# Kernel optimization log

Hardware: AMD Instinct MI355X
Metric: run time of the kernel (lower is better)

## Reference

```python
import jax, jax.numpy as jnp
import numpy as np

B, S, M = 8, 2048, 2048
STATE, MEM, DH, DOUT = 1024, 1024, 512, 512
K_CURV = 1.0
BETA = 1.0 / np.sqrt(DH)
EPS = 1e-12
MAX_TAN_NORM = 3.5


def setup_inputs() -> dict:
    key = jax.random.key(0)
    ks = jax.random.split(key, 6)
    return {
        "queries": jax.random.normal(ks[0], (B, S, STATE), jnp.float32),
        "keys": jax.random.normal(ks[1], (B, M, MEM), jnp.float32),
        "values": jax.random.normal(ks[2], (B, M, MEM), jnp.float32),
        "Wq": jax.random.normal(ks[3], (DH, STATE), jnp.float32) * (1.0 / np.sqrt(STATE)),
        "bq": jnp.zeros((DH,), jnp.float32),
        "Wk": jax.random.normal(ks[4], (DH, MEM), jnp.float32) * (1.0 / np.sqrt(MEM)),
        "bk": jnp.zeros((DH,), jnp.float32),
        "Wv": jax.random.normal(ks[5], (DOUT, MEM), jnp.float32) * (1.0 / np.sqrt(MEM)),
        "bv": jnp.zeros((DOUT,), jnp.float32),
    }


def _expmap0(x, k):
    # to_tangent0: [0, x] with norm clamped to <= 3.5 (time component is 0 so norm == ||x||)
    n = jnp.linalg.norm(x, axis=-1, keepdims=True)
    v = x * jnp.minimum(MAX_TAN_NORM / (n + 1e-7), 1.0)
    # exp map at origin o = (1/sqrt(k), 0) of Lorentz model with <x,x>_L = -1/k
    sk = jnp.sqrt(k)
    vn = jnp.maximum(jnp.linalg.norm(v, axis=-1, keepdims=True), EPS)
    th = sk * vn
    x0 = jnp.cosh(th) / sk
    xs = jnp.sinh(th) * v / (sk * vn)
    return jnp.concatenate([x0, xs], axis=-1)  # (..., d+1)


def _forward(queries, keys, values, Wq, bq, Wk, bk, Wv, bv):
    k = jnp.asarray(K_CURV, queries.dtype)
    sk = jnp.sqrt(k)
    Q = _expmap0(queries @ Wq.T + bq, k)  # (B,S,DH+1)
    Kh = _expmap0(keys @ Wk.T + bk, k)    # (B,M,DH+1)
    V = _expmap0(values @ Wv.T + bv, k)   # (B,M,DOUT+1)

    # pairwise Lorentz distance: d(x,y) = arccosh(-k <x,y>_L)/sqrt(k)
    # <x,y>_L = -x0*y0 + xs.ys ; computed as matmul + rank-1 term, no (B,S,M,d) blowup
    inner = jnp.einsum('bsd,bmd->bsm', Q[..., 1:], Kh[..., 1:]) \
            - Q[..., 0][:, :, None] * Kh[..., 0][:, None, :]
    dists = jnp.arccosh(jnp.maximum(-k * inner, 1.0 + 1e-7)) / sk  # (B,S,M)

    alpha = jax.nn.softmax(-BETA * dists, axis=-1)  # (B,S,M)

    # Einstein midpoint aggregation
    v_klein = V[..., 1:] / jnp.maximum(V[..., :1], EPS)                 # (B,M,DOUT)
    vn2 = jnp.minimum(jnp.sum(v_klein * v_klein, -1, keepdims=True), 1.0 - 1e-6)
    gamma = 1.0 / jnp.sqrt(jnp.maximum(1.0 - vn2, EPS))                 # (B,M,1)
    denom = jnp.maximum(jnp.einsum('bsm,bm->bs', alpha, gamma[..., 0]), EPS)[..., None]
    mid = jnp.einsum('bsm,bmd->bsd', alpha, gamma * v_klein) / denom    # (B,S,DOUT)
    mn = jnp.maximum(jnp.linalg.norm(mid, axis=-1, keepdims=True), EPS)
    mid = jnp.where(mn >= 1.0, mid / mn * (1.0 - 1e-6), mid)

    # Klein -> hyperboloid
    mn2 = jnp.minimum(jnp.sum(mid * mid, -1, keepdims=True), 1.0 - 1e-6)
    z0 = 1.0 / jnp.sqrt(jnp.maximum(k * (1.0 - mn2), EPS))
    zs = z0 * mid

    # logmap0 -> Euclidean spatial components
    d0 = jnp.arccosh(jnp.maximum(sk * z0, 1.0 + 1e-7)) / sk
    zsn = jnp.maximum(jnp.linalg.norm(zs, axis=-1, keepdims=True), EPS)
    return d0 * zs / zsn  # (B,S,DOUT)


def reference(queries, keys, values, Wq, bq, Wk, bk, Wv, bv):
    return _forward(queries, keys, values, Wq, bq, Wk, bk, Wv, bv)
```

## Files before the change

kernel.cpp:

```cpp
#include <hip/hip_runtime.h>
#include <hip/hip_bf16.h>
#include <cstdint>
#include <cstddef>


typedef _Float16 f16x8 __attribute__((ext_vector_type(8)));
typedef _Float16 f16x4 __attribute__((ext_vector_type(4)));
typedef float    f32x4 __attribute__((ext_vector_type(4)));

#define BETA_F 0.04419417382415922f
#define LOG2E_F 1.4426950408889634f
#define LN2_F 0.6931471805599453f

__device__ __forceinline__ void gload_lds16(const void* g, void* l) {
  __builtin_amdgcn_global_load_lds(
      (__attribute__((address_space(1))) void*)(g),
      (__attribute__((address_space(3))) void*)(l), 16, 0, 0);
}

#define K1_PIT 40

__global__ __launch_bounds__(256) void k_proj(
    const float* __restrict__ xq, const float* __restrict__ xk, const float* __restrict__ xv,
    const float* __restrict__ wq, const float* __restrict__ wk, const float* __restrict__ wv,
    const float* __restrict__ bq, const float* __restrict__ bk, const float* __restrict__ bv,
    _Float16* __restrict__ proj)
{
  __shared__ __align__(16) _Float16 As[128 * K1_PIT];
  __shared__ __align__(16) _Float16 Bs[128 * K1_PIT];

  const int tid = threadIdx.x;
  const int w = tid >> 6, l = tid & 63, ln = l & 15, q = l >> 4;
  const int wm = w & 1, wn = w >> 1;
  const int r0 = blockIdx.y * 128;
  const int n0 = blockIdx.x * 128;
  const int which = r0 >> 14;
  const int rloc = r0 & 16383;
  const float* X = (which == 0) ? xq : ((which == 1) ? xk : xv);
  const float* W = (which == 0) ? wq : ((which == 1) ? wk : wv);
  const float* bias = (which == 0) ? bq : ((which == 1) ? bk : bv);

  f32x4 acc[4][4];
#pragma unroll
  for (int mt = 0; mt < 4; ++mt)
#pragma unroll
    for (int nt = 0; nt < 4; ++nt) acc[mt][nt] = f32x4{0.f, 0.f, 0.f, 0.f};

  for (int kk = 0; kk < 1024; kk += 32) {
    __syncthreads();
#pragma unroll
    for (int it = 0; it < 4; ++it) {
      int v = tid + 256 * it;
      int row = v >> 3, c4 = v & 7;
      float4 a = *(const float4*)(X + (size_t)(rloc + row) * 1024 + kk + c4 * 4);
      float4 b = *(const float4*)(W + (size_t)(n0 + row) * 1024 + kk + c4 * 4);
      f16x4 ah = { (_Float16)a.x, (_Float16)a.y, (_Float16)a.z, (_Float16)a.w };
      f16x4 bh = { (_Float16)b.x, (_Float16)b.y, (_Float16)b.z, (_Float16)b.w };
      *(f16x4*)&As[row * K1_PIT + c4 * 4] = ah;
      *(f16x4*)&Bs[row * K1_PIT + c4 * 4] = bh;
    }
    __syncthreads();

    f16x8 af[4], bf[4];
#pragma unroll
    for (int mt = 0; mt < 4; ++mt)
      af[mt] = *(const f16x8*)&As[(wm * 64 + mt * 16 + ln) * K1_PIT + q * 8];
#pragma unroll
    for (int nt = 0; nt < 4; ++nt)
      bf[nt] = *(const f16x8*)&Bs[(wn * 64 + nt * 16 + ln) * K1_PIT + q * 8];
#pragma unroll
    for (int mt = 0; mt < 4; ++mt)
#pragma unroll
      for (int nt = 0; nt < 4; ++nt)
        acc[mt][nt] = __builtin_amdgcn_mfma_f32_16x16x32_f16(af[mt], bf[nt], acc[mt][nt], 0, 0, 0);
  }

  float bl[4];
#pragma unroll
  for (int nt = 0; nt < 4; ++nt) bl[nt] = bias[n0 + wn * 64 + nt * 16 + ln];
#pragma unroll
  for (int mt = 0; mt < 4; ++mt)
#pragma unroll
    for (int nt = 0; nt < 4; ++nt)
#pragma unroll
      for (int i = 0; i < 4; ++i) {
        int r = r0 + wm * 64 + mt * 16 + q * 4 + i;
        int c = n0 + wn * 64 + nt * 16 + ln;
        proj[(size_t)r * 512 + c] = (_Float16)(acc[mt][nt][i] + bl[nt]);
      }
}

__global__ __launch_bounds__(256) void k_rowstats(
    const _Float16* __restrict__ proj, float* __restrict__ fs, float* __restrict__ c0)
{
  const int w = threadIdx.x >> 6, l = threadIdx.x & 63;
  const int r = blockIdx.x * 4 + w;
  const f16x8 v = *(const f16x8*)(proj + (size_t)r * 512 + l * 8);
  float ss = 0.f;
#pragma unroll
  for (int j = 0; j < 8; ++j) { float x = (float)v[j]; ss += x * x; }
#pragma unroll
  for (int m = 1; m < 64; m <<= 1) ss += __shfl_xor(ss, m, 64);
  if (l == 0) {
    float n = sqrtf(ss);
    float s = fminf(3.5f / (n + 1e-7f), 1.0f);
    float vn = fmaxf(n * s, 1e-12f);
    float e = __builtin_amdgcn_exp2f(vn * LOG2E_F);
    float ie = 1.0f / e;
    c0[r] = 0.5f * (e + ie);
    fs[r] = 0.5f * (e - ie) * s / vn;
  }
}

#define K2_TP 72

__global__ __launch_bounds__(256) void k_transpose_v(
    const _Float16* __restrict__ proj, _Float16* __restrict__ xvT)
{
  __shared__ __align__(16) unsigned short t[64 * K2_TP];
  const int b = blockIdx.z, m0 = blockIdx.x * 64, d0 = blockIdx.y * 64;
  const unsigned short* pv =
      (const unsigned short*)(proj + (size_t)(32768 + b * 2048 + m0) * 512);
#pragma unroll
  for (int it = 0; it < 2; ++it) {
    int v = threadIdx.x + 256 * it;
    int r = v >> 3, c4 = v & 7;
    uint4 dd = *(const uint4*)(pv + (size_t)r * 512 + d0 + c4 * 8);
    *(uint4*)&t[r * K2_TP + c4 * 8] = dd;
  }
  __syncthreads();
#pragma unroll
  for (int it = 0; it < 2; ++it) {
    int v = threadIdx.x + 256 * it;
    int dr = v >> 3, mc = v & 7;
    unsigned int o[4];
#pragma unroll
    for (int jj = 0; jj < 4; ++jj) {
      unsigned int lo = t[(mc * 8 + jj * 2) * K2_TP + dr];
      unsigned int hi = t[(mc * 8 + jj * 2 + 1) * K2_TP + dr];
      o[jj] = lo | (hi << 16);
    }
    uint4 dd = { o[0], o[1], o[2], o[3] };
    unsigned short* dst =
        (unsigned short*)(xvT + ((size_t)b * 512 + d0 + dr) * 2048 + m0 + mc * 8);
    *(uint4*)dst = dd;
  }
}

__global__ __launch_bounds__(256, 2) void k_attn(
    const _Float16* __restrict__ proj, const _Float16* __restrict__ xvT,
    const float* __restrict__ fs, const float* __restrict__ c0,
    float* __restrict__ out)
{
  __shared__ __align__(16) _Float16 KV[16384];
  __shared__ __align__(16) _Float16 P[32 * 40];
  __shared__ float s_den[2][32];
  __shared__ float s_mn2[4][32];
  __shared__ float s_g[32];

  const int tid = threadIdx.x;
  const int w = tid >> 6, l = tid & 63, ln = l & 15, q = l >> 4;
  const int rh = w >> 1, ch = w & 1;
  const int b = blockIdx.y;
  const int s0 = blockIdx.x * 32;

  const _Float16* projq = proj + (size_t)(b * 2048 + s0) * 512;
  const _Float16* projk = proj + (size_t)(16384 + b * 2048) * 512;
  const _Float16* vt = xvT + (size_t)b * 512 * 2048;
  const float* fqp = fs + b * 2048 + s0;
  const float* fkp = fs + 16384 + b * 2048;
  const float* fvp = fs + 32768 + b * 2048;
  const float* cqp = c0 + b * 2048 + s0;
  const float* ckp = c0 + 16384 + b * 2048;
  const float* cvp = c0 + 32768 + b * 2048;

  f16x8 qf[16];
  {
    const _Float16* qrow = projq + (size_t)(rh * 16 + ln) * 512;
#pragma unroll
    for (int kc = 0; kc < 16; ++kc) qf[kc] = *(const f16x8*)(qrow + kc * 32 + q * 8);
  }
  float cq_i[4], fq_i[4];
#pragma unroll
  for (int i = 0; i < 4; ++i) {
    cq_i[i] = cqp[rh * 16 + q * 4 + i];
    fq_i[i] = fqp[rh * 16 + q * 4 + i];
  }

  f32x4 acc[2][8];
#pragma unroll
  for (int rt = 0; rt < 2; ++rt)
#pragma unroll
    for (int nt = 0; nt < 8; ++nt) acc[rt][nt] = f32x4{0.f, 0.f, 0.f, 0.f};
  float den_acc[4] = {0.f, 0.f, 0.f, 0.f};

  for (int m0 = 0; m0 < 2048; m0 += 32) {
    __syncthreads();
#pragma unroll
    for (int rr = 0; rr < 8; ++rr) {
      int mloc = w * 8 + rr;
      const _Float16* g = projk + (size_t)(m0 + mloc) * 512 + ((l ^ (mloc & 7)) * 8);
      gload_lds16(g, &KV[mloc * 512]);
    }
    const int mla = m0 + ch * 16 + ln;
    const float ck_v = ckp[mla], fk_v = fkp[mla], fv_v = fvp[mla], cv_v = cvp[mla];
    __syncthreads();

    f32x4 pacc = f32x4{0.f, 0.f, 0.f, 0.f};
    {
      const _Float16* krow = &KV[(ch * 16 + ln) * 512];
      const int msw = (ch * 16 + ln) & 7;
#pragma unroll
      for (int kc = 0; kc < 16; ++kc) {
        f16x8 kf = *(const f16x8*)(krow + (((kc * 4 + q) ^ msw) * 8));
        pacc = __builtin_amdgcn_mfma_f32_16x16x32_f16(qf[kc], kf, pacc, 0, 0, 0);
      }
    }
#pragma unroll
    for (int i = 0; i < 4; ++i) {
      float x = cq_i[i] * ck_v - (fq_i[i] * fk_v) * pacc[i];
      x = fmaxf(x, 1.0f + 1e-7f);
      float r_ = x + __builtin_amdgcn_sqrtf(x * x - 1.0f);
      float p = __builtin_amdgcn_exp2f(-BETA_F * __builtin_amdgcn_logf(r_));
      den_acc[i] += p * cv_v;
      P[(rh * 16 + q * 4 + i) * 40 + ch * 16 + ln] = (_Float16)(p * fv_v);
    }
    __syncthreads();
#pragma unroll
    for (int uu = 0; uu < 8; ++uu) {
      int u = w * 8 + uu;
      int dloc = u * 16 + (l >> 2);
      int cg = (l & 3) ^ ((dloc >> 1) & 3);
      const _Float16* g = vt + (size_t)dloc * 2048 + m0 + cg * 8;
      gload_lds16(g, &KV[u * 512]);
    }
    __syncthreads();
#pragma unroll
    for (int rt = 0; rt < 2; ++rt) {
      f16x8 pf = *(const f16x8*)&P[(rt * 16 + ln) * 40 + q * 8];
#pragma unroll
      for (int nt = 0; nt < 8; ++nt) {
        int d = w * 128 + nt * 16 + ln;
        f16x8 vf = *(const f16x8*)&KV[d * 32 + ((q ^ ((d >> 1) & 3)) * 8)];
        acc[rt][nt] = __builtin_amdgcn_mfma_f32_16x16x32_f16(pf, vf, acc[rt][nt], 0, 0, 0);
      }
    }
  }

#pragma unroll
  for (int i = 0; i < 4; ++i) {
    float v = den_acc[i];
    v += __shfl_xor(v, 1, 64); v += __shfl_xor(v, 2, 64);
    v += __shfl_xor(v, 4, 64); v += __shfl_xor(v, 8, 64);
    if (ln == 0) s_den[ch][rh * 16 + q * 4 + i] = v;
  }
  __syncthreads();
  if (tid < 32) {
    float dv = fmaxf(s_den[0][tid] + s_den[1][tid], 1e-12f);
    s_den[0][tid] = 1.0f / dv;
  }
  __syncthreads();
#pragma unroll
  for (int rt = 0; rt < 2; ++rt)
#pragma unroll
    for (int i = 0; i < 4; ++i) {
      int s = rt * 16 + q * 4 + i;
      float inv = s_den[0][s];
      float mm = 0.f;
#pragma unroll
      for (int nt = 0; nt < 8; ++nt) {
        float mid = acc[rt][nt][i] * inv;
        mm += mid * mid;
      }
      mm += __shfl_xor(mm, 1, 64); mm += __shfl_xor(mm, 2, 64);
      mm += __shfl_xor(mm, 4, 64); mm += __shfl_xor(mm, 8, 64);
      if (ln == 0) s_mn2[w][s] = mm;
    }
  __syncthreads();
  if (tid < 32) {
    float mn2 = s_mn2[0][tid] + s_mn2[1][tid] + s_mn2[2][tid] + s_mn2[3][tid];
    float mn = sqrtf(mn2);
    float sc = (mn >= 1.0f) ? (1.0f - 1e-6f) / mn : 1.0f;
    float mn2c = fminf(mn2 * sc * sc, 1.0f - 1e-6f);
    float z0 = 1.0f / sqrtf(fmaxf(1.0f - mn2c, 1e-12f));
    float zc = fmaxf(z0, 1.0f + 1e-7f);
    float d0 = LN2_F * __builtin_amdgcn_logf(zc + __builtin_amdgcn_sqrtf(zc * zc - 1.0f));
    s_g[tid] = (d0 / fmaxf(mn, 1e-12f)) * s_den[0][tid];
  }
  __syncthreads();

  float* pbuf = (float*)KV;
  for (int sp = 0; sp < 16; ++sp) {
#pragma unroll
    for (int rt = 0; rt < 2; ++rt)
#pragma unroll
      for (int i = 0; i < 4; ++i) {
        int s = rt * 16 + q * 4 + i;
        if ((s >> 1) == sp) {
          float gg = s_g[s];
#pragma unroll
          for (int nt = 0; nt < 8; ++nt)
            pbuf[(s & 1) * 512 + w * 128 + nt * 16 + ln] = gg * acc[rt][nt][i];
        }
      }
    __syncthreads();
    {
      int row = tid >> 7, c4 = tid & 127;
      float4 vv = *(float4*)&pbuf[row * 512 + c4 * 4];
      *(float4*)&out[((size_t)(b * 2048 + s0 + sp * 2 + row)) * 512 + c4 * 4] = vv;
    }
    __syncthreads();
  }
}

extern "C" void kernel_launch(void* const* d_in, const int* in_sizes, int n_in,
                              void* d_out, int out_size, void* d_ws, size_t ws_size,
                              hipStream_t stream) {
  (void)in_sizes; (void)n_in; (void)out_size; (void)ws_size;
  const float* xq = (const float*)d_in[0];
  const float* xk = (const float*)d_in[1];
  const float* xv = (const float*)d_in[2];
  const float* wq = (const float*)d_in[3];
  const float* bq = (const float*)d_in[4];
  const float* wk = (const float*)d_in[5];
  const float* bk = (const float*)d_in[6];
  const float* wv = (const float*)d_in[7];
  const float* bv = (const float*)d_in[8];
  float* out = (float*)d_out;
  char* ws = (char*)d_ws;

  _Float16* proj = (_Float16*)(ws);
  _Float16* xvT  = (_Float16*)(ws + 50331648);
  float* fsc     = (float*)(ws + 67108864);
  float* c0a     = (float*)(ws + 67305472);

  k_proj<<<dim3(4, 384), 256, 0, stream>>>(xq, xk, xv, wq, wk, wv, bq, bk, bv, proj);
  k_rowstats<<<dim3(12288), 256, 0, stream>>>(proj, fsc, c0a);
  k_transpose_v<<<dim3(32, 8, 8), 256, 0, stream>>>(proj, xvT);
  k_attn<<<dim3(64, 8), 256, 0, stream>>>(proj, xvT, fsc, c0a, out);
}
```

Baseline: 479.6 us.

## Restructure projection and attention kernels with fp16 weights and fused row stats

A separate kernel now casts the weight matrices to fp16 once. The projection kernel uses 512 threads per block to cover all 512 output columns of a 128-row tile. It loads weights into LDS asynchronously with an XOR swizzle and computes the row norms and expmap coefficients in its epilogue, which removes the separate rowstats kernel. The attention kernel processes 64 keys per iteration with each wave owning 16 keys across both query subtiles, reads K and V fragments straight from global memory instead of staging them in LDS, double-buffers the P tile, and packs the coefficients as float2. The aim is fewer launches, less fp32 weight traffic and fewer barriers, at the cost of uncoalesced direct global reads for K and V.

```diff
diff --git a/kernel.cpp b/kernel.cpp
--- a/kernel.cpp
+++ b/kernel.cpp
@@ -18,97 +18,120 @@
       (__attribute__((address_space(3))) void*)(l), 16, 0, 0);
 }
 
-#define K1_PIT 40
-
-__global__ __launch_bounds__(256) void k_proj(
+__global__ __launch_bounds__(256) void k_wcast(
+    const float* __restrict__ wq, const float* __restrict__ wk,
+    const float* __restrict__ wv, _Float16* __restrict__ Wh)
+{
+  const int a = blockIdx.y;
+  const float* src = (a == 0) ? wq : ((a == 1) ? wk : wv);
+  const int idx = (blockIdx.x * 256 + threadIdx.x) * 8;
+  float4 v0 = *(const float4*)(src + idx);
+  float4 v1 = *(const float4*)(src + idx + 4);
+  f16x8 h = { (_Float16)v0.x, (_Float16)v0.y, (_Float16)v0.z, (_Float16)v0.w,
+              (_Float16)v1.x, (_Float16)v1.y, (_Float16)v1.z, (_Float16)v1.w };
+  *(f16x8*)(Wh + (size_t)a * 524288 + idx) = h;
+}
+
+#define APIT 72
+
+__global__ __launch_bounds__(512, 2) void k_proj(
     const float* __restrict__ xq, const float* __restrict__ xk, const float* __restrict__ xv,
-    const float* __restrict__ wq, const float* __restrict__ wk, const float* __restrict__ wv,
+    const _Float16* __restrict__ Wh,
     const float* __restrict__ bq, const float* __restrict__ bk, const float* __restrict__ bv,
-    _Float16* __restrict__ proj)
+    _Float16* __restrict__ proj, float2* __restrict__ fc2)
 {
-  __shared__ __align__(16) _Float16 As[128 * K1_PIT];
-  __shared__ __align__(16) _Float16 Bs[128 * K1_PIT];
+  __shared__ __align__(16) _Float16 As[128 * APIT];
+  __shared__ __align__(16) _Float16 Bs[512 * 64];
+  __shared__ float ssq[128];
 
   const int tid = threadIdx.x;
   const int w = tid >> 6, l = tid & 63, ln = l & 15, q = l >> 4;
   const int wm = w & 1, wn = w >> 1;
-  const int r0 = blockIdx.y * 128;
-  const int n0 = blockIdx.x * 128;
+  const int r0 = blockIdx.x * 128;
   const int which = r0 >> 14;
   const int rloc = r0 & 16383;
   const float* X = (which == 0) ? xq : ((which == 1) ? xk : xv);
-  const float* W = (which == 0) ? wq : ((which == 1) ? wk : wv);
+  const _Float16* Whb = Wh + (size_t)which * 524288;
   const float* bias = (which == 0) ? bq : ((which == 1) ? bk : bv);
 
-  f32x4 acc[4][4];
+  if (tid < 128) ssq[tid] = 0.f;
+
+  f32x4 acc[4][8];
 #pragma unroll
   for (int mt = 0; mt < 4; ++mt)
 #pragma unroll
-    for (int nt = 0; nt < 4; ++nt) acc[mt][nt] = f32x4{0.f, 0.f, 0.f, 0.f};
-
-  for (int kk = 0; kk < 1024; kk += 32) {
-    __syncthreads();
-#pragma unroll
-    for (int it = 0; it < 4; ++it) {
-      int v = tid + 256 * it;
-      int row = v >> 3, c4 = v & 7;
-      float4 a = *(const float4*)(X + (size_t)(rloc + row) * 1024 + kk + c4 * 4);
-      float4 b = *(const float4*)(W + (size_t)(n0 + row) * 1024 + kk + c4 * 4);
-      f16x4 ah = { (_Float16)a.x, (_Float16)a.y, (_Float16)a.z, (_Float16)a.w };
-      f16x4 bh = { (_Float16)b.x, (_Float16)b.y, (_Float16)b.z, (_Float16)b.w };
-      *(f16x4*)&As[row * K1_PIT + c4 * 4] = ah;
-      *(f16x4*)&Bs[row * K1_PIT + c4 * 4] = bh;
-    }
-    __syncthreads();
-
-    f16x8 af[4], bf[4];
-#pragma unroll
-    for (int mt = 0; mt < 4; ++mt)
-      af[mt] = *(const f16x8*)&As[(wm * 64 + mt * 16 + ln) * K1_PIT + q * 8];
-#pragma unroll
-    for (int nt = 0; nt < 4; ++nt)
-      bf[nt] = *(const f16x8*)&Bs[(wn * 64 + nt * 16 + ln) * K1_PIT + q * 8];
-#pragma unroll
-    for (int mt = 0; mt < 4; ++mt)
-#pragma unroll
-      for (int nt = 0; nt < 4; ++nt)
-        acc[mt][nt] = __builtin_amdgcn_mfma_f32_16x16x32_f16(af[mt], bf[nt], acc[mt][nt], 0, 0, 0);
-  }
-
-  float bl[4];
-#pragma unroll
-  for (int nt = 0; nt < 4; ++nt) bl[nt] = bias[n0 + wn * 64 + nt * 16 + ln];
+    for (int nt = 0; nt < 8; ++nt) acc[mt][nt] = f32x4{0.f, 0.f, 0.f, 0.f};
+
+  const int arow = tid >> 2, akq = tid & 3;
+  for (int kk = 0; kk < 1024; kk += 64) {
+    __syncthreads();
+    {
+      const float* xp = X + (size_t)(rloc + arow) * 1024 + kk + akq * 16;
+      float4 a0 = *(const float4*)(xp);
+      float4 a1 = *(const float4*)(xp + 4);
+      float4 a2 = *(const float4*)(xp + 8);
+      float4 a3 = *(const float4*)(xp + 12);
+      f16x8 h0 = { (_Float16)a0.x, (_Float16)a0.y, (_Float16)a0.z, (_Float16)a0.w,
+                   (_Float16)a1.x, (_Float16)a1.y, (_Float16)a1.z, (_Float16)a1.w };
+      f16x8 h1 = { (_Float16)a2.x, (_Float16)a2.y, (_Float16)a2.z, (_Float16)a2.w,
+                   (_Float16)a3.x, (_Float16)a3.y, (_Float16)a3.z, (_Float16)a3.w };
+      *(f16x8*)&As[arow * APIT + akq * 16] = h0;
+      *(f16x8*)&As[arow * APIT + akq * 16 + 8] = h1;
+    }
+#pragma unroll
+    for (int j = 0; j < 8; ++j) {
+      int u = w * 8 + j;
+      int row = u * 8 + (l >> 3);
+      int cg = (l & 7) ^ (row & 7);
+      gload_lds16(Whb + (size_t)row * 1024 + kk + cg * 8, &Bs[u * 512]);
+    }
+    __syncthreads();
+#pragma unroll
+    for (int kc = 0; kc < 2; ++kc) {
+      f16x8 af[4], bf[8];
+#pragma unroll
+      for (int mt = 0; mt < 4; ++mt)
+        af[mt] = *(const f16x8*)&As[(wm * 64 + mt * 16 + ln) * APIT + kc * 32 + q * 8];
+#pragma unroll
+      for (int nt = 0; nt < 8; ++nt) {
+        int row = wn * 128 + nt * 16 + ln;
+        bf[nt] = *(const f16x8*)&Bs[row * 64 + (((kc * 4 + q) ^ (row & 7)) * 8)];
+      }
+#pragma unroll
+      for (int mt = 0; mt < 4; ++mt)
+#pragma unroll
+        for (int nt = 0; nt < 8; ++nt)
+          acc[mt][nt] = __builtin_amdgcn_mfma_f32_16x16x32_f16(af[mt], bf[nt], acc[mt][nt], 0, 0, 0);
+    }
+  }
+
+  float bl[8];
+#pragma unroll
+  for (int nt = 0; nt < 8; ++nt) bl[nt] = bias[wn * 128 + nt * 16 + ln];
 #pragma unroll
   for (int mt = 0; mt < 4; ++mt)
 #pragma unroll
-    for (int nt = 0; nt < 4; ++nt)
-#pragma unroll
-      for (int i = 0; i < 4; ++i) {
-        int r = r0 + wm * 64 + mt * 16 + q * 4 + i;
-        int c = n0 + wn * 64 + nt * 16 + ln;
-        proj[(size_t)r * 512 + c] = (_Float16)(acc[mt][nt][i] + bl[nt]);
-      }
-}
-
-__global__ __launch_bounds__(256) void k_rowstats(
-    const _Float16* __restrict__ proj, float* __restrict__ fs, float* __restrict__ c0)
-{
-  const int w = threadIdx.x >> 6, l = threadIdx.x & 63;
-  const int r = blockIdx.x * 4 + w;
-  const f16x8 v = *(const f16x8*)(proj + (size_t)r * 512 + l * 8);
-  float ss = 0.f;
-#pragma unroll
-  for (int j = 0; j < 8; ++j) { float x = (float)v[j]; ss += x * x; }
-#pragma unroll
-  for (int m = 1; m < 64; m <<= 1) ss += __shfl_xor(ss, m, 64);
-  if (l == 0) {
-    float n = sqrtf(ss);
+    for (int i = 0; i < 4; ++i) {
+      float ss = 0.f;
+#pragma unroll
+      for (int nt = 0; nt < 8; ++nt) {
+        float v = acc[mt][nt][i] + bl[nt];
+        proj[(size_t)(r0 + wm * 64 + mt * 16 + q * 4 + i) * 512 + wn * 128 + nt * 16 + ln] =
+            (_Float16)v;
+        ss += v * v;
+      }
+      ss += __shfl_xor(ss, 1, 64); ss += __shfl_xor(ss, 2, 64);
+      ss += __shfl_xor(ss, 4, 64); ss += __shfl_xor(ss, 8, 64);
+      if (ln == 0) atomicAdd(&ssq[wm * 64 + mt * 16 + q * 4 + i], ss);
+    }
+  __syncthreads();
+  if (tid < 128) {
+    float n = sqrtf(ssq[tid]);
     float s = fminf(3.5f / (n + 1e-7f), 1.0f);
     float vn = fmaxf(n * s, 1e-12f);
     float e = __builtin_amdgcn_exp2f(vn * LOG2E_F);
     float ie = 1.0f / e;
-    c0[r] = 0.5f * (e + ie);
-    fs[r] = 0.5f * (e - ie) * s / vn;
+    fc2[r0 + tid] = make_float2(0.5f * (e + ie), 0.5f * (e - ie) * s / vn);
   }
 }
 
@@ -147,129 +170,123 @@
   }
 }
 
+#define PPIT 72
+
 __global__ __launch_bounds__(256, 2) void k_attn(
     const _Float16* __restrict__ proj, const _Float16* __restrict__ xvT,
-    const float* __restrict__ fs, const float* __restrict__ c0,
-    float* __restrict__ out)
+    const float2* __restrict__ fc2, float* __restrict__ out)
 {
-  __shared__ __align__(16) _Float16 KV[16384];
-  __shared__ __align__(16) _Float16 P[32 * 40];
-  __shared__ float s_den[2][32];
+  __shared__ __align__(16) _Float16 P[2][32 * PPIT];
+  __shared__ float s_den[4][32];
   __shared__ float s_mn2[4][32];
   __shared__ float s_g[32];
 
   const int tid = threadIdx.x;
   const int w = tid >> 6, l = tid & 63, ln = l & 15, q = l >> 4;
-  const int rh = w >> 1, ch = w & 1;
-  const int b = blockIdx.y;
-  const int s0 = blockIdx.x * 32;
+  const int blk = blockIdx.x;
+  const int b = blk & 7;
+  const int s0 = (blk >> 3) * 32;
 
   const _Float16* projq = proj + (size_t)(b * 2048 + s0) * 512;
   const _Float16* projk = proj + (size_t)(16384 + b * 2048) * 512;
   const _Float16* vt = xvT + (size_t)b * 512 * 2048;
-  const float* fqp = fs + b * 2048 + s0;
-  const float* fkp = fs + 16384 + b * 2048;
-  const float* fvp = fs + 32768 + b * 2048;
-  const float* cqp = c0 + b * 2048 + s0;
-  const float* ckp = c0 + 16384 + b * 2048;
-  const float* cvp = c0 + 32768 + b * 2048;
-
-  f16x8 qf[16];
-  {
-    const _Float16* qrow = projq + (size_t)(rh * 16 + ln) * 512;
-#pragma unroll
-    for (int kc = 0; kc < 16; ++kc) qf[kc] = *(const f16x8*)(qrow + kc * 32 + q * 8);
-  }
-  float cq_i[4], fq_i[4];
-#pragma unroll
-  for (int i = 0; i < 4; ++i) {
-    cq_i[i] = cqp[rh * 16 + q * 4 + i];
-    fq_i[i] = fqp[rh * 16 + q * 4 + i];
-  }
+  const float2* fcq = fc2 + b * 2048 + s0;
+  const float2* fck = fc2 + 16384 + b * 2048;
+  const float2* fcv = fc2 + 32768 + b * 2048;
+
+  f16x8 qf[2][16];
+#pragma unroll
+  for (int st = 0; st < 2; ++st) {
+    const _Float16* qrow = projq + (size_t)(st * 16 + ln) * 512 + q * 8;
+#pragma unroll
+    for (int kc = 0; kc < 16; ++kc) qf[st][kc] = *(const f16x8*)(qrow + kc * 32);
+  }
+  float cq_i[2][4], fq_i[2][4];
+#pragma unroll
+  for (int st = 0; st < 2; ++st)
+#pragma unroll
+    for (int i = 0; i < 4; ++i) {
+      float2 t = fcq[st * 16 + q * 4 + i];
+      cq_i[st][i] = t.x; fq_i[st][i] = t.y;
+    }
 
   f32x4 acc[2][8];
 #pragma unroll
-  for (int rt = 0; rt < 2; ++rt)
-#pragma unroll
-    for (int nt = 0; nt < 8; ++nt) acc[rt][nt] = f32x4{0.f, 0.f, 0.f, 0.f};
-  float den_acc[4] = {0.f, 0.f, 0.f, 0.f};
-
-  for (int m0 = 0; m0 < 2048; m0 += 32) {
-    __syncthreads();
-#pragma unroll
-    for (int rr = 0; rr < 8; ++rr) {
-      int mloc = w * 8 + rr;
-      const _Float16* g = projk + (size_t)(m0 + mloc) * 512 + ((l ^ (mloc & 7)) * 8);
-      gload_lds16(g, &KV[mloc * 512]);
-    }
-    const int mla = m0 + ch * 16 + ln;
-    const float ck_v = ckp[mla], fk_v = fkp[mla], fv_v = fvp[mla], cv_v = cvp[mla];
-    __syncthreads();
-
-    f32x4 pacc = f32x4{0.f, 0.f, 0.f, 0.f};
+  for (int st = 0; st < 2; ++st)
+#pragma unroll
+    for (int dt = 0; dt < 8; ++dt) acc[st][dt] = f32x4{0.f, 0.f, 0.f, 0.f};
+  float den_acc[2][4] = {{0.f,0.f,0.f,0.f},{0.f,0.f,0.f,0.f}};
+
+  for (int it = 0; it < 32; ++it) {
+    const int m0 = it * 64;
+    _Float16* Pc = P[it & 1];
+    const int mla = m0 + w * 16 + ln;
+
+    f32x4 pacc0 = f32x4{0.f,0.f,0.f,0.f}, pacc1 = f32x4{0.f,0.f,0.f,0.f};
     {
-      const _Float16* krow = &KV[(ch * 16 + ln) * 512];
-      const int msw = (ch * 16 + ln) & 7;
+      const _Float16* krow = projk + (size_t)mla * 512 + q * 8;
 #pragma unroll
       for (int kc = 0; kc < 16; ++kc) {
-        f16x8 kf = *(const f16x8*)(krow + (((kc * 4 + q) ^ msw) * 8));
-        pacc = __builtin_amdgcn_mfma_f32_16x16x32_f16(qf[kc], kf, pacc, 0, 0, 0);
-      }
-    }
+        f16x8 kf = *(const f16x8*)(krow + kc * 32);
+        pacc0 = __builtin_amdgcn_mfma_f32_16x16x32_f16(qf[0][kc], kf, pacc0, 0, 0, 0);
+        pacc1 = __builtin_amdgcn_mfma_f32_16x16x32_f16(qf[1][kc], kf, pacc1, 0, 0, 0);
+      }
+    }
+    float2 ks = fck[mla];
+    float2 vs = fcv[mla];
+#pragma unroll
+    for (int st = 0; st < 2; ++st) {
+      const f32x4& pa = st ? pacc1 : pacc0;
+#pragma unroll
+      for (int i = 0; i < 4; ++i) {
+        float x = cq_i[st][i] * ks.x - (fq_i[st][i] * ks.y) * pa[i];
+        x = fmaxf(x, 1.0f + 1e-7f);
+        float r_ = x + __builtin_amdgcn_sqrtf(x * x - 1.0f);
+        float p = __builtin_amdgcn_exp2f(-BETA_F * __builtin_amdgcn_logf(r_));
+        den_acc[st][i] += p * vs.x;
+        Pc[(st * 16 + q * 4 + i) * PPIT + w * 16 + ln] = (_Float16)(p * vs.y);
+      }
+    }
+    __syncthreads();
+#pragma unroll
+    for (int kc2 = 0; kc2 < 2; ++kc2) {
+      f16x8 pf0 = *(const f16x8*)&Pc[(ln) * PPIT + kc2 * 32 + q * 8];
+      f16x8 pf1 = *(const f16x8*)&Pc[(16 + ln) * PPIT + kc2 * 32 + q * 8];
+      const _Float16* vb = vt + (size_t)(w * 128 + ln) * 2048 + m0 + kc2 * 32 + q * 8;
+#pragma unroll
+      for (int dt = 0; dt < 8; ++dt) {
+        f16x8 vf = *(const f16x8*)(vb + (size_t)dt * 16 * 2048);
+        acc[0][dt] = __builtin_amdgcn_mfma_f32_16x16x32_f16(pf0, vf, acc[0][dt], 0, 0, 0);
+        acc[1][dt] = __builtin_amdgcn_mfma_f32_16x16x32_f16(pf1, vf, acc[1][dt], 0, 0, 0);
+      }
+    }
+  }
+
+#pragma unroll
+  for (int st = 0; st < 2; ++st)
 #pragma unroll
     for (int i = 0; i < 4; ++i) {
-      float x = cq_i[i] * ck_v - (fq_i[i] * fk_v) * pacc[i];
-      x = fmaxf(x, 1.0f + 1e-7f);
-      float r_ = x + __builtin_amdgcn_sqrtf(x * x - 1.0f);
-      float p = __builtin_amdgcn_exp2f(-BETA_F * __builtin_amdgcn_logf(r_));
-      den_acc[i] += p * cv_v;
-      P[(rh * 16 + q * 4 + i) * 40 + ch * 16 + ln] = (_Float16)(p * fv_v);
-    }
-    __syncthreads();
-#pragma unroll
-    for (int uu = 0; uu < 8; ++uu) {
-      int u = w * 8 + uu;
-      int dloc = u * 16 + (l >> 2);
-      int cg = (l & 3) ^ ((dloc >> 1) & 3);
-      const _Float16* g = vt + (size_t)dloc * 2048 + m0 + cg * 8;
-      gload_lds16(g, &KV[u * 512]);
-    }
-    __syncthreads();
-#pragma unroll
-    for (int rt = 0; rt < 2; ++rt) {
-      f16x8 pf = *(const f16x8*)&P[(rt * 16 + ln) * 40 + q * 8];
-#pragma unroll
-      for (int nt = 0; nt < 8; ++nt) {
-        int d = w * 128 + nt * 16 + ln;
-        f16x8 vf = *(const f16x8*)&KV[d * 32 + ((q ^ ((d >> 1) & 3)) * 8)];
-        acc[rt][nt] = __builtin_amdgcn_mfma_f32_16x16x32_f16(pf, vf, acc[rt][nt], 0, 0, 0);
-      }
-    }
-  }
-
-#pragma unroll
-  for (int i = 0; i < 4; ++i) {
-    float v = den_acc[i];
-    v += __shfl_xor(v, 1, 64); v += __shfl_xor(v, 2, 64);
-    v += __shfl_xor(v, 4, 64); v += __shfl_xor(v, 8, 64);
-    if (ln == 0) s_den[ch][rh * 16 + q * 4 + i] = v;
-  }
+      float v = den_acc[st][i];
+      v += __shfl_xor(v, 1, 64); v += __shfl_xor(v, 2, 64);
+      v += __shfl_xor(v, 4, 64); v += __shfl_xor(v, 8, 64);
+      if (ln == 0) s_den[w][st * 16 + q * 4 + i] = v;
+    }
   __syncthreads();
   if (tid < 32) {
-    float dv = fmaxf(s_den[0][tid] + s_den[1][tid], 1e-12f);
+    float dv = fmaxf(s_den[0][tid] + s_den[1][tid] + s_den[2][tid] + s_den[3][tid], 1e-12f);
     s_den[0][tid] = 1.0f / dv;
   }
   __syncthreads();
 #pragma unroll
-  for (int rt = 0; rt < 2; ++rt)
+  for (int st = 0; st < 2; ++st)
 #pragma unroll
     for (int i = 0; i < 4; ++i) {
-      int s = rt * 16 + q * 4 + i;
+      int s = st * 16 + q * 4 + i;
       float inv = s_den[0][s];
       float mm = 0.f;
 #pragma unroll
-      for (int nt = 0; nt < 8; ++nt) {
-        float mid = acc[rt][nt][i] * inv;
+      for (int dt = 0; dt < 8; ++dt) {
+        float mid = acc[st][dt][i] * inv;
         mm += mid * mid;
       }
       mm += __shfl_xor(mm, 1, 64); mm += __shfl_xor(mm, 2, 64);
@@ -289,18 +306,18 @@
   }
   __syncthreads();
 
-  float* pbuf = (float*)KV;
+  float* pbuf = (float*)P;
   for (int sp = 0; sp < 16; ++sp) {
 #pragma unroll
-    for (int rt = 0; rt < 2; ++rt)
+    for (int st = 0; st < 2; ++st)
 #pragma unroll
       for (int i = 0; i < 4; ++i) {
-        int s = rt * 16 + q * 4 + i;
+        int s = st * 16 + q * 4 + i;
         if ((s >> 1) == sp) {
           float gg = s_g[s];
 #pragma unroll
-          for (int nt = 0; nt < 8; ++nt)
-            pbuf[(s & 1) * 512 + w * 128 + nt * 16 + ln] = gg * acc[rt][nt][i];
+          for (int dt = 0; dt < 8; ++dt)
+            pbuf[(s & 1) * 512 + w * 128 + dt * 16 + ln] = gg * acc[st][dt][i];
         }
       }
     __syncthreads();
@@ -330,12 +347,12 @@
   char* ws = (char*)d_ws;
 
   _Float16* proj = (_Float16*)(ws);
+  _Float16* Wh   = (_Float16*)(ws + 50331648);
   _Float16* xvT  = (_Float16*)(ws + 50331648);
-  float* fsc     = (float*)(ws + 67108864);
-  float* c0a     = (float*)(ws + 67305472);
-
-  k_proj<<<dim3(4, 384), 256, 0, stream>>>(xq, xk, xv, wq, wk, wv, bq, bk, bv, proj);
-  k_rowstats<<<dim3(12288), 256, 0, stream>>>(proj, fsc, c0a);
+  float2* fc2    = (float2*)(ws + 67108864);
+
+  k_wcast<<<dim3(256, 3), 256, 0, stream>>>(wq, wk, wv, Wh);
+  k_proj<<<dim3(384), 512, 0, stream>>>(xq, xk, xv, Wh, bq, bk, bv, proj, fc2);
   k_transpose_v<<<dim3(32, 8, 8), 256, 0, stream>>>(proj, xvT);
-  k_attn<<<dim3(64, 8), 256, 0, stream>>>(proj, xvT, fsc, c0a, out);
-}
+  k_attn<<<dim3(512), 256, 0, stream>>>(proj, xvT, fc2, out);
+}
```

After: 593.5 us. 1.24x slower.
